# Optimization experiments

Measured on AMD Instinct MI355X. Metric: run time of the kernel, lower is better.

Reference implementation:

```python
import jax, jax.numpy as jnp
import numpy as np

B, N, E = 2, 5000, 160000
F_IN, HID, ED = 128, 128, 16
IN_EDGE = 2 * F_IN + 16 + ED  # source, target, radial(4*4), edge_attr


def _lin(k, fan_in, fan_out):
    return (jax.random.normal(k, (fan_in, fan_out), jnp.float32) / np.sqrt(fan_in)).astype(jnp.float32)


def setup_inputs() -> dict:
    key = jax.random.key(0)
    ks = jax.random.split(key, 16)
    h = jax.random.normal(ks[0], (B, N, F_IN), jnp.float32)
    coord = jax.random.normal(ks[1], (B, N, 4, 3), jnp.float32)
    edge_index = jax.random.randint(ks[2], (2, E), 0, N)
    edge_attr = jax.random.normal(ks[3], (E, ED), jnp.float32)
    return {
        "h": h, "coord": coord, "edge_index": edge_index, "edge_attr": edge_attr,
        # edge_mlp: Linear(IN_EDGE->HID), ReLU, Linear(HID->HID), ReLU
        "W_e1": _lin(ks[4], IN_EDGE, HID), "b_e1": jnp.zeros((HID,), jnp.float32),
        "W_e2": _lin(ks[5], HID, HID), "b_e2": jnp.zeros((HID,), jnp.float32),
        # node_mlp: Linear(HID+F_IN->HID), ReLU, Linear(HID->F_IN)
        "W_n1": _lin(ks[6], HID + F_IN, HID), "b_n1": jnp.zeros((HID,), jnp.float32),
        "W_n2": _lin(ks[7], HID, F_IN), "b_n2": jnp.zeros((F_IN,), jnp.float32),
        # coord_mlp: Linear(HID->HID), ReLU, Linear(HID->4, bias=False, xavier gain 0.001)
        "W_c1": _lin(ks[8], HID, HID), "b_c1": jnp.zeros((HID,), jnp.float32),
        "W_c2": _lin(ks[9], HID, 4) * 0.001,
    }


def reference(h, coord, edge_index, edge_attr,
              W_e1, b_e1, W_e2, b_e2,
              W_n1, b_n1, W_n2, b_n2,
              W_c1, b_c1, W_c2):
    row, col = edge_index[0], edge_index[1]
    coords_weight = 1.0
    n_nodes = h.shape[1]

    def single(h_b, coord_b):
        # coord2radial
        cd = coord_b[row] - coord_b[col]                                  # [E,4,3]
        prod = jnp.einsum('ejt,ekt->ejk', cd, cd).reshape(cd.shape[0], -1)  # [E,16]
        nrm = jnp.linalg.norm(prod, axis=-1, keepdims=True)
        radial = prod / jnp.maximum(nrm, 1e-12)                           # F.normalize
        # edge_model
        x = jnp.concatenate([h_b[row], h_b[col], radial, edge_attr], axis=-1)
        ef = jax.nn.relu(jax.nn.relu(x @ W_e1 + b_e1) @ W_e2 + b_e2)      # [E,HID]
        # coord_model: segment mean of cd * coord_mlp(ef)
        w = jax.nn.relu(ef @ W_c1 + b_c1) @ W_c2                          # [E,4]
        trans = cd * w[:, :, None]                                        # [E,4,3]
        agg_c = jax.ops.segment_sum(trans, row, num_segments=n_nodes)     # [N,4,3]
        cnt = jax.ops.segment_sum(jnp.ones((row.shape[0],), trans.dtype), row,
                                  num_segments=n_nodes)                   # [N]
        coord_new = coord_b + (agg_c / jnp.maximum(cnt, 1.0)[:, None, None]) * coords_weight
        # node_model (recurrent)
        agg_h = jax.ops.segment_sum(ef, row, num_segments=n_nodes)        # [N,HID]
        z = jnp.concatenate([h_b, agg_h], axis=-1)
        h_new = h_b + jax.nn.relu(z @ W_n1 + b_n1) @ W_n2 + b_n2
        return h_new, coord_new

    hs, coords = jax.vmap(single)(h, coord)
    return hs, coords
```

## Files before the change

### kernel.cpp

```cpp
#include <hip/hip_runtime.h>
#include <hip/hip_bf16.h>

#define B   2
#define NN_ 5000
#define NE_ 160000
#define F   128
#define HID 128
#define ED  16

typedef __bf16 bf16x8 __attribute__((ext_vector_type(8)));
typedef __bf16 bf16x4 __attribute__((ext_vector_type(4)));
typedef float  f32x4  __attribute__((ext_vector_type(4)));

#define MS  136
#define PS  40
#define EDG 64
#define ZS  264
#define HS  136
#define NPB2 32
#define NBUCKET 313

__global__ void pack_hist_kernel(const float* __restrict__ We1, const float* __restrict__ We2,
                                 const float* __restrict__ Wc1, const float* __restrict__ Wc2,
                                 const float* __restrict__ Wn1, const float* __restrict__ Wn2,
                                 const int* __restrict__ ei,
                                 __bf16* __restrict__ pw1, __bf16* __restrict__ pw2,
                                 __bf16* __restrict__ pwc1, __bf16* __restrict__ pwc2,
                                 __bf16* __restrict__ pwn1, __bf16* __restrict__ pwn2,
                                 float4* __restrict__ agg4, int* __restrict__ csr_cnt)
{
    if (blockIdx.x >= 472) {
        int i = (blockIdx.x - 472) * 256 + threadIdx.x;
        if (i < NE_) atomicAdd(&csr_cnt[ei[i]], 1);
        return;
    }
    int idx = blockIdx.x * 256 + threadIdx.x;
    const float* W; __bf16* P; int KT, Nr, local;
    if (idx < 36864)       { W = We1; P = pw1;  KT = 9; Nr = 128; local = idx; }
    else if (idx < 53248)  { W = We2; P = pw2;  KT = 4; Nr = 128; local = idx - 36864; }
    else if (idx < 69632)  { W = Wc1; P = pwc1; KT = 4; Nr = 128; local = idx - 53248; }
    else if (idx < 71680)  { W = Wc2; P = pwc2; KT = 4; Nr = 4;   local = idx - 69632; }
    else if (idx < 104448) { W = Wn1; P = pwn1; KT = 8; Nr = 128; local = idx - 71680; }
    else                   { W = Wn2; P = pwn2; KT = 4; Nr = 128; local = idx - 104448; }
    int j = local & 7, lane = (local >> 3) & 63, rest = local >> 9;
    int kt = rest % KT, nt = rest / KT;
    int k = kt * 32 + (lane >> 4) * 8 + j;
    int n = nt * 16 + (lane & 15);
    float v = (n < Nr) ? W[k * Nr + n] : 0.f;
    P[local] = (__bf16)v;

    float4 z4 = {0.f, 0.f, 0.f, 0.f};
    for (int i = idx; i < 350000; i += 120832) agg4[i] = z4;
}

__global__ __launch_bounds__(512) void scan_kernel(const int* __restrict__ csr_cnt,
                                                   int* __restrict__ csr_off, int* __restrict__ csr_pos)
{
    __shared__ int part[512];
    const int t = threadIdx.x;
    int sum = 0;
    #pragma unroll
    for (int j = 0; j < 10; j++) {
        int idx = t * 10 + j;
        if (idx < NN_) sum += csr_cnt[idx];
    }
    part[t] = sum;
    __syncthreads();
    for (int off = 1; off < 512; off <<= 1) {
        int v = (t >= off) ? part[t - off] : 0;
        __syncthreads();
        part[t] += v;
        __syncthreads();
    }
    int run = part[t] - sum;
    #pragma unroll
    for (int j = 0; j < 10; j++) {
        int idx = t * 10 + j;
        if (idx < NN_) { csr_off[idx] = run; csr_pos[idx] = run; run += csr_cnt[idx]; }
    }
    if (t == 0) csr_off[NN_] = NE_;
}

__global__ __launch_bounds__(512) void mid_kernel(
    const int* __restrict__ ei,
    int* __restrict__ csr_pos, int* __restrict__ bucket,
    const float* __restrict__ h, const __bf16* __restrict__ pw1,
    const float* __restrict__ be1,
    __bf16* __restrict__ pr, __bf16* __restrict__ pc)
{
    __shared__ __align__(16) __bf16 hs[128 * MS];
    const int t = threadIdx.x;

    if (blockIdx.x < NBUCKET) {
        int i = blockIdx.x * 512 + t;
        if (i < NE_) {
            int p = atomicAdd(&csr_pos[ei[i]], 1);
            bucket[p] = i;
        }
        return;
    }

    const int bp = blockIdx.x - NBUCKET;
    const int b = bp / 40;
    const int n0 = (bp % 40) * 128;
    const int lane = t & 63, wave = t >> 6;
    const int quad = lane >> 4, c = lane & 15;

    #pragma unroll
    for (int it = 0; it < 8; it++) {
        int idx = it * 512 + t;
        int node = idx >> 5, ch = idx & 31;
        int gn = n0 + node;
        float4 v = (gn < NN_) ? *(const float4*)&h[((size_t)b * NN_ + gn) * F + ch * 4]
                              : (float4){0.f, 0.f, 0.f, 0.f};
        bf16x4 bv = {(__bf16)v.x, (__bf16)v.y, (__bf16)v.z, (__bf16)v.w};
        *(bf16x4*)&hs[node * MS + ch * 4] = bv;
    }
    __syncthreads();

    const bf16x8* pw1v = (const bf16x8*)pw1;
    f32x4 accr[8], accc[8];
    #pragma unroll
    for (int m = 0; m < 8; m++) { accr[m] = (f32x4){0,0,0,0}; accc[m] = (f32x4){0,0,0,0}; }
    for (int kt = 0; kt < 4; kt++) {
        bf16x8 wr = pw1v[(wave * 9 + kt) * 64 + lane];
        bf16x8 wc = pw1v[(wave * 9 + kt + 4) * 64 + lane];
        #pragma unroll
        for (int m = 0; m < 8; m++) {
            bf16x8 x = *(const bf16x8*)&hs[(m * 16 + c) * MS + kt * 32 + quad * 8];
            accr[m] = __builtin_amdgcn_mfma_f32_16x16x32_bf16(wr, x, accr[m], 0, 0, 0);
            accc[m] = __builtin_amdgcn_mfma_f32_16x16x32_bf16(wc, x, accc[m], 0, 0, 0);
        }
    }
    float4 bb = *(const float4*)&be1[wave * 16 + quad * 4];
    #pragma unroll
    for (int m = 0; m < 8; m++) {
        int gn = n0 + m * 16 + c;
        if (gn < NN_) {
            size_t base = ((size_t)b * NN_ + gn) * F + wave * 16 + quad * 4;
            bf16x4 orr = {(__bf16)(accr[m][0] + bb.x), (__bf16)(accr[m][1] + bb.y),
                          (__bf16)(accr[m][2] + bb.z), (__bf16)(accr[m][3] + bb.w)};
            bf16x4 occ = {(__bf16)accc[m][0], (__bf16)accc[m][1], (__bf16)accc[m][2], (__bf16)accc[m][3]};
            *(bf16x4*)&pr[base] = orr;
            *(bf16x4*)&pc[base] = occ;
        }
    }
}

__global__ __launch_bounds__(256, 4) void edge_kernel(
    const __bf16* __restrict__ pr, const __bf16* __restrict__ pc,
    const float* __restrict__ coord,
    const int* __restrict__ ei, const float* __restrict__ ea,
    const int* __restrict__ bucket,
    const float* __restrict__ be2, const float* __restrict__ bc1,
    const __bf16* __restrict__ pw1, const __bf16* __restrict__ pw2,
    const __bf16* __restrict__ pwc1, const __bf16* __restrict__ pwc2,
    float* __restrict__ agg_h, float* __restrict__ agg_c)
{
    __shared__ __align__(16) __bf16 buf1[EDG * MS];
    __shared__ __align__(16) __bf16 buf2[EDG * MS];
    __shared__ __bf16 cds[EDG][12];
    __shared__ int rs[EDG], cs[EDG];

    const int t = threadIdx.x;
    const int b = blockIdx.y;
    const int p0 = blockIdx.x * EDG;
    const int lane = t & 63, wave = t >> 6;
    const int quad = lane >> 4, c = lane & 15;

    int eid_reg = 0;
    if (t < EDG) {
        eid_reg = bucket[p0 + t];
        rs[t] = ei[eid_reg]; cs[t] = ei[NE_ + eid_reg];
    }
    __syncthreads();

    const __bf16* prb = pr + (size_t)b * NN_ * F;
    const __bf16* pcb = pc + (size_t)b * NN_ * F;
    #pragma unroll
    for (int it = 0; it < 4; it++) {
        int idx = it * 256 + t;
        int e = idx >> 4, ch = idx & 15;
        bf16x8 a = *(const bf16x8*)(prb + (size_t)rs[e] * F + ch * 8);
        bf16x8 v = *(const bf16x8*)(pcb + (size_t)cs[e] * F + ch * 8);
        bf16x8 o;
        #pragma unroll
        for (int j = 0; j < 8; j++) o[j] = (__bf16)((float)a[j] + (float)v[j]);
        *(bf16x8*)&buf1[e * MS + ch * 8] = o;
    }
    if (t < EDG) {
        int e = t;
        const float* cr = coord + ((size_t)b * NN_ + rs[e]) * 12;
        const float* cc = coord + ((size_t)b * NN_ + cs[e]) * 12;
        float cd[12];
        #pragma unroll
        for (int j = 0; j < 12; j++) { cd[j] = cr[j] - cc[j]; cds[e][j] = (__bf16)cd[j]; }
        float prod[16]; float ss = 0.f;
        #pragma unroll
        for (int j = 0; j < 4; j++)
            #pragma unroll
            for (int k = 0; k < 4; k++) {
                float p = cd[j*3]*cd[k*3] + cd[j*3+1]*cd[k*3+1] + cd[j*3+2]*cd[k*3+2];
                prod[j*4 + k] = p; ss += p * p;
            }
        float inv = 1.0f / fmaxf(sqrtf(ss), 1e-12f);
        #pragma unroll
        for (int j = 0; j < 16; j++) buf2[e * PS + j] = (__bf16)(prod[j] * inv);
        const float4* ep = (const float4*)(ea + (size_t)eid_reg * ED);
        #pragma unroll
        for (int j = 0; j < 4; j++) {
            float4 v = ep[j];
            bf16x4 bv = {(__bf16)v.x, (__bf16)v.y, (__bf16)v.z, (__bf16)v.w};
            *(bf16x4*)&buf2[e * PS + 16 + j * 4] = bv;
        }
    }
    __syncthreads();

    const bf16x8* pw1v  = (const bf16x8*)pw1;
    const bf16x8* pw2v  = (const bf16x8*)pw2;
    const bf16x8* pwc1v = (const bf16x8*)pwc1;
    const bf16x8* pwc2v = (const bf16x8*)pwc2;

    f32x4 acc1[4][2];
    #pragma unroll
    for (int m = 0; m < 4; m++)
        #pragma unroll
        for (int n = 0; n < 2; n++) acc1[m][n] = (f32x4){0,0,0,0};
    {
        bf16x8 x1[4];
        #pragma unroll
        for (int m = 0; m < 4; m++)
            x1[m] = *(const bf16x8*)&buf2[(m*16 + c) * PS + quad*8];
        #pragma unroll
        for (int n = 0; n < 2; n++) {
            bf16x8 w = pw1v[((2*wave + n)*9 + 8)*64 + lane];
            #pragma unroll
            for (int m = 0; m < 4; m++)
                acc1[m][n] = __builtin_amdgcn_mfma_f32_16x16x32_bf16(w, x1[m], acc1[m][n], 0, 0, 0);
        }
    }
    #pragma unroll
    for (int n = 0; n < 2; n++) {
        int nt = 2*wave + n;
        #pragma unroll
        for (int m = 0; m < 4; m++) {
            int row = m*16 + c;
            bf16x4 p = *(const bf16x4*)&buf1[row * MS + nt*16 + quad*4];
            bf16x4 o = { (__bf16)fmaxf(acc1[m][n][0] + (float)p[0], 0.f),
                         (__bf16)fmaxf(acc1[m][n][1] + (float)p[1], 0.f),
                         (__bf16)fmaxf(acc1[m][n][2] + (float)p[2], 0.f),
                         (__bf16)fmaxf(acc1[m][n][3] + (float)p[3], 0.f) };
            *(bf16x4*)&buf1[row * MS + nt*16 + quad*4] = o;
        }
    }
    __syncthreads();

    f32x4 acc2[4][2];
    #pragma unroll
    for (int m = 0; m < 4; m++)
        #pragma unroll
        for (int n = 0; n < 2; n++) acc2[m][n] = (f32x4){0,0,0,0};
    for (int kt = 0; kt < 4; kt++) {
        bf16x8 x[4];
        #pragma unroll
        for (int m = 0; m < 4; m++)
            x[m] = *(const bf16x8*)&buf1[(m*16 + c) * MS + kt*32 + quad*8];
        #pragma unroll
        for (int n = 0; n < 2; n++) {
            bf16x8 w = pw2v[((2*wave + n)*4 + kt)*64 + lane];
            #pragma unroll
            for (int m = 0; m < 4; m++)
                acc2[m][n] = __builtin_amdgcn_mfma_f32_16x16x32_bf16(w, x[m], acc2[m][n], 0, 0, 0);
        }
    }
    #pragma unroll
    for (int n = 0; n < 2; n++) {
        int nt = 2*wave + n;
        float4 bb = *(const float4*)&be2[nt*16 + quad*4];
        #pragma unroll
        for (int m = 0; m < 4; m++) {
            int row = m*16 + c;
            bf16x4 o = { (__bf16)fmaxf(acc2[m][n][0] + bb.x, 0.f),
                         (__bf16)fmaxf(acc2[m][n][1] + bb.y, 0.f),
                         (__bf16)fmaxf(acc2[m][n][2] + bb.z, 0.f),
                         (__bf16)fmaxf(acc2[m][n][3] + bb.w, 0.f) };
            *(bf16x4*)&buf2[row * MS + nt*16 + quad*4] = o;
        }
    }
    __syncthreads();

    f32x4 acc3[4][2];
    #pragma unroll
    for (int m = 0; m < 4; m++)
        #pragma unroll
        for (int n = 0; n < 2; n++) acc3[m][n] = (f32x4){0,0,0,0};
    for (int kt = 0; kt < 4; kt++) {
        bf16x8 x[4];
        #pragma unroll
        for (int m = 0; m < 4; m++)
            x[m] = *(const bf16x8*)&buf2[(m*16 + c) * MS + kt*32 + quad*8];
        #pragma unroll
        for (int n = 0; n < 2; n++) {
            bf16x8 w = pwc1v[((2*wave + n)*4 + kt)*64 + lane];
            #pragma unroll
            for (int m = 0; m < 4; m++)
                acc3[m][n] = __builtin_amdgcn_mfma_f32_16x16x32_bf16(w, x[m], acc3[m][n], 0, 0, 0);
        }
    }
    #pragma unroll
    for (int n = 0; n < 2; n++) {
        int nt = 2*wave + n;
        float4 bb = *(const float4*)&bc1[nt*16 + quad*4];
        #pragma unroll
        for (int m = 0; m < 4; m++) {
            int row = m*16 + c;
            bf16x4 o = { (__bf16)fmaxf(acc3[m][n][0] + bb.x, 0.f),
                         (__bf16)fmaxf(acc3[m][n][1] + bb.y, 0.f),
                         (__bf16)fmaxf(acc3[m][n][2] + bb.z, 0.f),
                         (__bf16)fmaxf(acc3[m][n][3] + bb.w, 0.f) };
            *(bf16x4*)&buf1[row * MS + nt*16 + quad*4] = o;
        }
    }
    __syncthreads();

    f32x4 accw = (f32x4){0,0,0,0};
    for (int kt = 0; kt < 4; kt++) {
        bf16x8 x = *(const bf16x8*)&buf1[(wave*16 + c) * MS + kt*32 + quad*8];
        accw = __builtin_amdgcn_mfma_f32_16x16x32_bf16(pwc2v[kt*64 + lane], x, accw, 0, 0, 0);
    }
    if (quad == 0) {
        int e = wave*16 + c;
        #pragma unroll
        for (int j = 0; j < 12; j++)
            cds[e][j] = (__bf16)((float)cds[e][j] * accw[j/3]);
    }

    {
        float* aggh_b = agg_h + (size_t)b * NN_ * HID;
        const int col = t & 127, seg = t >> 7;
        float run = 0.f;
        int cur = rs[seg * 32];
        for (int e = seg * 32; e < seg * 32 + 32; e++) {
            int r = rs[e];
            float v = (float)buf2[e * MS + col];
            if (r != cur) {
                atomicAdd(&aggh_b[(size_t)cur * HID + col], run);
                run = 0.f; cur = r;
            }
            run += v;
        }
        atomicAdd(&aggh_b[(size_t)cur * HID + col], run);
    }
    __syncthreads();

    if (t < 24) {
        float* aggc_b = agg_c + (size_t)b * NN_ * 12;
        const int j = t % 12, q = t / 12;
        float run = 0.f;
        int cur = rs[q * 32];
        for (int e = q * 32; e < q * 32 + 32; e++) {
            int r = rs[e];
            float v = (float)cds[e][j];
            if (r != cur) {
                atomicAdd(&aggc_b[(size_t)cur * 12 + j], run);
                run = 0.f; cur = r;
            }
            run += v;
        }
        atomicAdd(&aggc_b[(size_t)cur * 12 + j], run);
    }
}

__global__ __launch_bounds__(256) void node_kernel(
    const float* __restrict__ h, const float* __restrict__ agg_h,
    const float* __restrict__ agg_c, const float* __restrict__ coord,
    const int* __restrict__ csr_off,
    const __bf16* __restrict__ pwn1, const float* __restrict__ bn1,
    const __bf16* __restrict__ pwn2, const float* __restrict__ bn2,
    float* __restrict__ out_h, float* __restrict__ out_c)
{
    __shared__ __align__(16) __bf16 zs[NPB2 * ZS];
    __shared__ __align__(16) __bf16 h1s[NPB2 * HS];
    const int t = threadIdx.x;
    const int b = blockIdx.y;
    const int n0 = blockIdx.x * NPB2;
    const int lane = t & 63, wave = t >> 6;
    const int quad = lane >> 4, c = lane & 15;

    #pragma unroll
    for (int it = 0; it < 8; it++) {
        int idx = it * 256 + t;
        int node = idx >> 6, ch = idx & 63;
        int gn = n0 + node;
        float4 v = (float4){0.f, 0.f, 0.f, 0.f};
        if (gn < NN_) {
            const float* src = (ch < 32) ? &h[((size_t)b * NN_ + gn) * F + ch * 4]
                                         : &agg_h[((size_t)b * NN_ + gn) * HID + (ch - 32) * 4];
            v = *(const float4*)src;
        }
        bf16x4 bv = {(__bf16)v.x, (__bf16)v.y, (__bf16)v.z, (__bf16)v.w};
        *(bf16x4*)&zs[node * ZS + ch * 4] = bv;
    }
    __syncthreads();

    const bf16x8* w1v = (const bf16x8*)pwn1;
    const bf16x8* w2v = (const bf16x8*)pwn2;
    f32x4 a1[2][2];
    #pragma unroll
    for (int m = 0; m < 2; m++)
        #pragma unroll
        for (int n = 0; n < 2; n++) a1[m][n] = (f32x4){0,0,0,0};
    for (int kt = 0; kt < 8; kt++) {
        bf16x8 x[2];
        #pragma unroll
        for (int m = 0; m < 2; m++)
            x[m] = *(const bf16x8*)&zs[(m*16 + c) * ZS + kt*32 + quad*8];
        #pragma unroll
        for (int n = 0; n < 2; n++) {
            bf16x8 w = w1v[((2*wave + n)*8 + kt)*64 + lane];
            #pragma unroll
            for (int m = 0; m < 2; m++)
                a1[m][n] = __builtin_amdgcn_mfma_f32_16x16x32_bf16(w, x[m], a1[m][n], 0, 0, 0);
        }
    }
    __syncthreads();
    #pragma unroll
    for (int n = 0; n < 2; n++) {
        int nt = 2*wave + n;
        float4 bb = *(const float4*)&bn1[nt*16 + quad*4];
        #pragma unroll
        for (int m = 0; m < 2; m++) {
            bf16x4 o = { (__bf16)fmaxf(a1[m][n][0] + bb.x, 0.f),
                         (__bf16)fmaxf(a1[m][n][1] + bb.y, 0.f),
                         (__bf16)fmaxf(a1[m][n][2] + bb.z, 0.f),
                         (__bf16)fmaxf(a1[m][n][3] + bb.w, 0.f) };
            *(bf16x4*)&h1s[(m*16 + c) * HS + nt*16 + quad*4] = o;
        }
    }
    __syncthreads();

    f32x4 a2[2][2];
    #pragma unroll
    for (int m = 0; m < 2; m++)
        #pragma unroll
        for (int n = 0; n < 2; n++) a2[m][n] = (f32x4){0,0,0,0};
    for (int kt = 0; kt < 4; kt++) {
        bf16x8 x[2];
        #pragma unroll
        for (int m = 0; m < 2; m++)
            x[m] = *(const bf16x8*)&h1s[(m*16 + c) * HS + kt*32 + quad*8];
        #pragma unroll
        for (int n = 0; n < 2; n++) {
            bf16x8 w = w2v[((2*wave + n)*4 + kt)*64 + lane];
            #pragma unroll
            for (int m = 0; m < 2; m++)
                a2[m][n] = __builtin_amdgcn_mfma_f32_16x16x32_bf16(w, x[m], a2[m][n], 0, 0, 0);
        }
    }
    float* os = (float*)zs;
    #pragma unroll
    for (int n = 0; n < 2; n++) {
        int nt = 2*wave + n;
        float4 bb = *(const float4*)&bn2[nt*16 + quad*4];
        #pragma unroll
        for (int m = 0; m < 2; m++) {
            f32x4 o = { a2[m][n][0] + bb.x, a2[m][n][1] + bb.y,
                        a2[m][n][2] + bb.z, a2[m][n][3] + bb.w };
            *(f32x4*)&os[(m*16 + c) * 132 + nt*16 + quad*4] = o;
        }
    }
    __syncthreads();

    #pragma unroll
    for (int it = 0; it < 4; it++) {
        int idx = it * 256 + t;
        int node = idx >> 5, ch = idx & 31;
        int gn = n0 + node;
        if (gn < NN_) {
            size_t gb = ((size_t)b * NN_ + gn) * F + ch * 4;
            float4 hres = *(const float4*)&h[gb];
            float4 acc = *(const float4*)&os[node * 132 + ch * 4];
            float4 o = { hres.x + acc.x, hres.y + acc.y, hres.z + acc.z, hres.w + acc.w };
            *(float4*)&out_h[gb] = o;
        }
    }
    for (int idx = t; idx < NPB2 * 12; idx += 256) {
        int node = idx / 12, j = idx % 12;
        int gn = n0 + node;
        if (gn < NN_) {
            float deg = (float)(csr_off[gn + 1] - csr_off[gn]);
            size_t ci = ((size_t)b * NN_ + gn) * 12 + j;
            out_c[ci] = coord[ci] + agg_c[ci] / fmaxf(deg, 1.0f);
        }
    }
}

extern "C" void kernel_launch(void* const* d_in, const int* in_sizes, int n_in,
                              void* d_out, int out_size, void* d_ws, size_t ws_size,
                              hipStream_t stream) {
    const float* h     = (const float*)d_in[0];
    const float* coord = (const float*)d_in[1];
    const int*   ei    = (const int*)d_in[2];
    const float* ea    = (const float*)d_in[3];
    const float* We1   = (const float*)d_in[4];
    const float* be1   = (const float*)d_in[5];
    const float* We2   = (const float*)d_in[6];
    const float* be2   = (const float*)d_in[7];
    const float* Wn1   = (const float*)d_in[8];
    const float* bn1   = (const float*)d_in[9];
    const float* Wn2   = (const float*)d_in[10];
    const float* bn2   = (const float*)d_in[11];
    const float* Wc1   = (const float*)d_in[12];
    const float* bc1   = (const float*)d_in[13];
    const float* Wc2   = (const float*)d_in[14];

    float* out_h = (float*)d_out;
    float* out_c = out_h + (size_t)B * NN_ * F;

    unsigned char* base = (unsigned char*)d_ws;
    __bf16* pw1  = (__bf16*)base;
    __bf16* pw2  = pw1 + 36864;
    __bf16* pwc1 = pw2 + 16384;
    __bf16* pwc2 = pwc1 + 16384;
    __bf16* pwn1 = pwc2 + 2048;
    __bf16* pwn2 = pwn1 + 32768;
    unsigned char* dyn = base + 241664;

    int* csr_cnt = (int*)(dyn);
    int* csr_off = (int*)(dyn + 20000);
    int* csr_pos = (int*)(dyn + 40016);
    int* bucket  = (int*)(dyn + 60016);
    float* agg_h = (float*)(dyn + 700016);
    float* agg_c = agg_h + (size_t)B * NN_ * HID;
    __bf16* pr   = (__bf16*)(agg_c + (size_t)B * NN_ * 12);
    __bf16* pc   = pr + (size_t)B * NN_ * F;

    hipMemsetAsync(csr_cnt, 0, 20000, stream);

    pack_hist_kernel<<<472 + 625, 256, 0, stream>>>(We1, We2, Wc1, Wc2, Wn1, Wn2, ei,
                                                    pw1, pw2, pwc1, pwc2, pwn1, pwn2,
                                                    (float4*)agg_h, csr_cnt);

    scan_kernel<<<1, 512, 0, stream>>>(csr_cnt, csr_off, csr_pos);

    mid_kernel<<<NBUCKET + 80, 512, 0, stream>>>(ei, csr_pos, bucket, h, pw1, be1, pr, pc);

    dim3 eg(NE_ / EDG, B);
    edge_kernel<<<eg, 256, 0, stream>>>(pr, pc, coord, ei, ea, bucket, be2, bc1,
                                        pw1, pw2, pwc1, pwc2, agg_h, agg_c);

    dim3 ng((NN_ + NPB2 - 1) / NPB2, B);
    node_kernel<<<ng, 256, 0, stream>>>(h, agg_h, agg_c, coord, csr_off,
                                        pwn1, bn1, pwn2, bn2, out_h, out_c);
}
```

Measured before the change: 193.5 us.

## Make edge kernel persistent with register prefetch of next chunk's gathers

The edge kernel becomes a persistent grid of 1024 blocks that loop over edge chunks. Each block prefetches the next chunk's bucket indices, projected node rows, coordinates and edge attributes into registers while the current chunk's MLP runs, so gather latency is hidden behind compute. The node projection (pr/pc) moves into the pack/histogram kernel, reading We1 directly from fp32 so it does not depend on the packed weights, and the bucket scatter becomes its own kernel. The coord2radial step is spread across 4 lanes per edge using shuffles. The cost is higher register pressure from the prefetch buffers and possible load imbalance across persistent blocks.

```diff
diff --git a/kernel.cpp b/kernel.cpp
--- a/kernel.cpp
+++ b/kernel.cpp
@@ -18,89 +18,50 @@
 #define ZS  264
 #define HS  136
 #define NPB2 32
-#define NBUCKET 313
-
-__global__ void pack_hist_kernel(const float* __restrict__ We1, const float* __restrict__ We2,
-                                 const float* __restrict__ Wc1, const float* __restrict__ Wc2,
-                                 const float* __restrict__ Wn1, const float* __restrict__ Wn2,
-                                 const int* __restrict__ ei,
-                                 __bf16* __restrict__ pw1, __bf16* __restrict__ pw2,
-                                 __bf16* __restrict__ pwc1, __bf16* __restrict__ pwc2,
-                                 __bf16* __restrict__ pwn1, __bf16* __restrict__ pwn2,
-                                 float4* __restrict__ agg4, int* __restrict__ csr_cnt)
-{
-    if (blockIdx.x >= 472) {
-        int i = (blockIdx.x - 472) * 256 + threadIdx.x;
-        if (i < NE_) atomicAdd(&csr_cnt[ei[i]], 1);
-        return;
-    }
-    int idx = blockIdx.x * 256 + threadIdx.x;
-    const float* W; __bf16* P; int KT, Nr, local;
-    if (idx < 36864)       { W = We1; P = pw1;  KT = 9; Nr = 128; local = idx; }
-    else if (idx < 53248)  { W = We2; P = pw2;  KT = 4; Nr = 128; local = idx - 36864; }
-    else if (idx < 69632)  { W = Wc1; P = pwc1; KT = 4; Nr = 128; local = idx - 53248; }
-    else if (idx < 71680)  { W = Wc2; P = pwc2; KT = 4; Nr = 4;   local = idx - 69632; }
-    else if (idx < 104448) { W = Wn1; P = pwn1; KT = 8; Nr = 128; local = idx - 71680; }
-    else                   { W = Wn2; P = pwn2; KT = 4; Nr = 128; local = idx - 104448; }
-    int j = local & 7, lane = (local >> 3) & 63, rest = local >> 9;
-    int kt = rest % KT, nt = rest / KT;
-    int k = kt * 32 + (lane >> 4) * 8 + j;
-    int n = nt * 16 + (lane & 15);
-    float v = (n < Nr) ? W[k * Nr + n] : 0.f;
-    P[local] = (__bf16)v;
-
-    float4 z4 = {0.f, 0.f, 0.f, 0.f};
-    for (int i = idx; i < 350000; i += 120832) agg4[i] = z4;
-}
-
-__global__ __launch_bounds__(512) void scan_kernel(const int* __restrict__ csr_cnt,
-                                                   int* __restrict__ csr_off, int* __restrict__ csr_pos)
-{
-    __shared__ int part[512];
-    const int t = threadIdx.x;
-    int sum = 0;
-    #pragma unroll
-    for (int j = 0; j < 10; j++) {
-        int idx = t * 10 + j;
-        if (idx < NN_) sum += csr_cnt[idx];
-    }
-    part[t] = sum;
-    __syncthreads();
-    for (int off = 1; off < 512; off <<= 1) {
-        int v = (t >= off) ? part[t - off] : 0;
-        __syncthreads();
-        part[t] += v;
-        __syncthreads();
-    }
-    int run = part[t] - sum;
-    #pragma unroll
-    for (int j = 0; j < 10; j++) {
-        int idx = t * 10 + j;
-        if (idx < NN_) { csr_off[idx] = run; csr_pos[idx] = run; run += csr_cnt[idx]; }
-    }
-    if (t == 0) csr_off[NN_] = NE_;
-}
-
-__global__ __launch_bounds__(512) void mid_kernel(
+#define EGRID 1024
+#define NCHUNK 5000
+
+__global__ __launch_bounds__(512) void pack_hist_kernel(
+    const float* __restrict__ We1, const float* __restrict__ We2,
+    const float* __restrict__ Wc1, const float* __restrict__ Wc2,
+    const float* __restrict__ Wn1, const float* __restrict__ Wn2,
     const int* __restrict__ ei,
-    int* __restrict__ csr_pos, int* __restrict__ bucket,
-    const float* __restrict__ h, const __bf16* __restrict__ pw1,
-    const float* __restrict__ be1,
+    const float* __restrict__ h, const float* __restrict__ be1,
+    __bf16* __restrict__ pw1, __bf16* __restrict__ pw2,
+    __bf16* __restrict__ pwc1, __bf16* __restrict__ pwc2,
+    __bf16* __restrict__ pwn1, __bf16* __restrict__ pwn2,
+    float4* __restrict__ agg4, int* __restrict__ csr_cnt,
     __bf16* __restrict__ pr, __bf16* __restrict__ pc)
 {
     __shared__ __align__(16) __bf16 hs[128 * MS];
     const int t = threadIdx.x;
 
-    if (blockIdx.x < NBUCKET) {
-        int i = blockIdx.x * 512 + t;
-        if (i < NE_) {
-            int p = atomicAdd(&csr_pos[ei[i]], 1);
-            bucket[p] = i;
-        }
+    if (blockIdx.x < 236) {
+        int idx = blockIdx.x * 512 + t;
+        const float* W; __bf16* P; int KT, Nr, local;
+        if (idx < 36864)       { W = We1; P = pw1;  KT = 9; Nr = 128; local = idx; }
+        else if (idx < 53248)  { W = We2; P = pw2;  KT = 4; Nr = 128; local = idx - 36864; }
+        else if (idx < 69632)  { W = Wc1; P = pwc1; KT = 4; Nr = 128; local = idx - 53248; }
+        else if (idx < 71680)  { W = Wc2; P = pwc2; KT = 4; Nr = 4;   local = idx - 69632; }
+        else if (idx < 104448) { W = Wn1; P = pwn1; KT = 8; Nr = 128; local = idx - 71680; }
+        else                   { W = Wn2; P = pwn2; KT = 4; Nr = 128; local = idx - 104448; }
+        int j = local & 7, lane = (local >> 3) & 63, rest = local >> 9;
+        int kt = rest % KT, nt = rest / KT;
+        int k = kt * 32 + (lane >> 4) * 8 + j;
+        int n = nt * 16 + (lane & 15);
+        float v = (n < Nr) ? W[k * Nr + n] : 0.f;
+        P[local] = (__bf16)v;
+        float4 z4 = {0.f, 0.f, 0.f, 0.f};
+        for (int i = idx; i < 350000; i += 120832) agg4[i] = z4;
         return;
     }
-
-    const int bp = blockIdx.x - NBUCKET;
+    if (blockIdx.x < 549) {
+        int i = (blockIdx.x - 236) * 512 + t;
+        if (i < NE_) atomicAdd(&csr_cnt[ei[i]], 1);
+        return;
+    }
+
+    const int bp = blockIdx.x - 549;
     const int b = bp / 40;
     const int n0 = (bp % 40) * 128;
     const int lane = t & 63, wave = t >> 6;
@@ -118,13 +79,17 @@
     }
     __syncthreads();
 
-    const bf16x8* pw1v = (const bf16x8*)pw1;
     f32x4 accr[8], accc[8];
     #pragma unroll
     for (int m = 0; m < 8; m++) { accr[m] = (f32x4){0,0,0,0}; accc[m] = (f32x4){0,0,0,0}; }
     for (int kt = 0; kt < 4; kt++) {
-        bf16x8 wr = pw1v[(wave * 9 + kt) * 64 + lane];
-        bf16x8 wc = pw1v[(wave * 9 + kt + 4) * 64 + lane];
+        bf16x8 wr, wc;
+        #pragma unroll
+        for (int jj = 0; jj < 8; jj++) {
+            int k = kt * 32 + quad * 8 + jj;
+            wr[jj] = (__bf16)We1[k * HID + wave * 16 + c];
+            wc[jj] = (__bf16)We1[(k + 128) * HID + wave * 16 + c];
+        }
         #pragma unroll
         for (int m = 0; m < 8; m++) {
             bf16x8 x = *(const bf16x8*)&hs[(m * 16 + c) * MS + kt * 32 + quad * 8];
@@ -144,6 +109,45 @@
             *(bf16x4*)&pr[base] = orr;
             *(bf16x4*)&pc[base] = occ;
         }
+    }
+}
+
+__global__ __launch_bounds__(512) void scan_kernel(const int* __restrict__ csr_cnt,
+                                                   int* __restrict__ csr_off, int* __restrict__ csr_pos)
+{
+    __shared__ int part[512];
+    const int t = threadIdx.x;
+    int sum = 0;
+    #pragma unroll
+    for (int j = 0; j < 10; j++) {
+        int idx = t * 10 + j;
+        if (idx < NN_) sum += csr_cnt[idx];
+    }
+    part[t] = sum;
+    __syncthreads();
+    for (int off = 1; off < 512; off <<= 1) {
+        int v = (t >= off) ? part[t - off] : 0;
+        __syncthreads();
+        part[t] += v;
+        __syncthreads();
+    }
+    int run = part[t] - sum;
+    #pragma unroll
+    for (int j = 0; j < 10; j++) {
+        int idx = t * 10 + j;
+        if (idx < NN_) { csr_off[idx] = run; csr_pos[idx] = run; run += csr_cnt[idx]; }
+    }
+    if (t == 0) csr_off[NN_] = NE_;
+}
+
+__global__ __launch_bounds__(512) void scatter_kernel(const int* __restrict__ ei,
+                                                      int* __restrict__ csr_pos,
+                                                      int* __restrict__ bucket)
+{
+    int i = blockIdx.x * 512 + threadIdx.x;
+    if (i < NE_) {
+        int p = atomicAdd(&csr_pos[ei[i]], 1);
+        bucket[p] = i;
     }
 }
 
@@ -161,213 +165,270 @@
     __shared__ __align__(16) __bf16 buf2[EDG * MS];
     __shared__ __bf16 cds[EDG][12];
     __shared__ int rs[EDG], cs[EDG];
+    __shared__ int rsN[EDG], csN[EDG], eidsN[EDG];
 
     const int t = threadIdx.x;
-    const int b = blockIdx.y;
-    const int p0 = blockIdx.x * EDG;
     const int lane = t & 63, wave = t >> 6;
     const int quad = lane >> 4, c = lane & 15;
-
-    int eid_reg = 0;
-    if (t < EDG) {
-        eid_reg = bucket[p0 + t];
-        rs[t] = ei[eid_reg]; cs[t] = ei[NE_ + eid_reg];
-    }
-    __syncthreads();
-
-    const __bf16* prb = pr + (size_t)b * NN_ * F;
-    const __bf16* pcb = pc + (size_t)b * NN_ * F;
-    #pragma unroll
-    for (int it = 0; it < 4; it++) {
-        int idx = it * 256 + t;
-        int e = idx >> 4, ch = idx & 15;
-        bf16x8 a = *(const bf16x8*)(prb + (size_t)rs[e] * F + ch * 8);
-        bf16x8 v = *(const bf16x8*)(pcb + (size_t)cs[e] * F + ch * 8);
-        bf16x8 o;
-        #pragma unroll
-        for (int j = 0; j < 8; j++) o[j] = (__bf16)((float)a[j] + (float)v[j]);
-        *(bf16x8*)&buf1[e * MS + ch * 8] = o;
-    }
-    if (t < EDG) {
-        int e = t;
-        const float* cr = coord + ((size_t)b * NN_ + rs[e]) * 12;
-        const float* cc = coord + ((size_t)b * NN_ + cs[e]) * 12;
-        float cd[12];
-        #pragma unroll
-        for (int j = 0; j < 12; j++) { cd[j] = cr[j] - cc[j]; cds[e][j] = (__bf16)cd[j]; }
-        float prod[16]; float ss = 0.f;
-        #pragma unroll
-        for (int j = 0; j < 4; j++)
-            #pragma unroll
-            for (int k = 0; k < 4; k++) {
-                float p = cd[j*3]*cd[k*3] + cd[j*3+1]*cd[k*3+1] + cd[j*3+2]*cd[k*3+2];
-                prod[j*4 + k] = p; ss += p * p;
-            }
-        float inv = 1.0f / fmaxf(sqrtf(ss), 1e-12f);
-        #pragma unroll
-        for (int j = 0; j < 16; j++) buf2[e * PS + j] = (__bf16)(prod[j] * inv);
-        const float4* ep = (const float4*)(ea + (size_t)eid_reg * ED);
-        #pragma unroll
-        for (int j = 0; j < 4; j++) {
-            float4 v = ep[j];
-            bf16x4 bv = {(__bf16)v.x, (__bf16)v.y, (__bf16)v.z, (__bf16)v.w};
-            *(bf16x4*)&buf2[e * PS + 16 + j * 4] = bv;
-        }
-    }
-    __syncthreads();
+    const int e4 = t >> 2, j4 = t & 3;
 
     const bf16x8* pw1v  = (const bf16x8*)pw1;
     const bf16x8* pw2v  = (const bf16x8*)pw2;
     const bf16x8* pwc1v = (const bf16x8*)pwc1;
     const bf16x8* pwc2v = (const bf16x8*)pwc2;
 
-    f32x4 acc1[4][2];
-    #pragma unroll
-    for (int m = 0; m < 4; m++)
-        #pragma unroll
-        for (int n = 0; n < 2; n++) acc1[m][n] = (f32x4){0,0,0,0};
+    int cid = blockIdx.x;
+
     {
-        bf16x8 x1[4];
+        const int bC = (cid >= 2500) ? 1 : 0;
+        const int p0 = (cid - bC * 2500) * EDG;
+        int mr = 0, mc = 0, me = 0;
+        if (t < EDG) {
+            me = bucket[p0 + t];
+            mr = ei[me];
+            mc = ei[NE_ + me];
+            rsN[t] = mr; csN[t] = mc; eidsN[t] = me;
+        }
+    }
+    __syncthreads();
+
+    bf16x8 prPF[4], pcPF[4];
+    float crN[3], ccN[3];
+    float4 eaNv;
+    {
+        const int bC = (cid >= 2500) ? 1 : 0;
+        const __bf16* prb = pr + (size_t)bC * NN_ * F;
+        const __bf16* pcb = pc + (size_t)bC * NN_ * F;
+        #pragma unroll
+        for (int it = 0; it < 4; it++) {
+            int idx = it * 256 + t, e = idx >> 4, ch = idx & 15;
+            prPF[it] = *(const bf16x8*)(prb + (size_t)rsN[e] * F + ch * 8);
+            pcPF[it] = *(const bf16x8*)(pcb + (size_t)csN[e] * F + ch * 8);
+        }
+        const float* crp = coord + ((size_t)bC * NN_ + rsN[e4]) * 12 + j4 * 3;
+        const float* ccp = coord + ((size_t)bC * NN_ + csN[e4]) * 12 + j4 * 3;
+        crN[0] = crp[0]; crN[1] = crp[1]; crN[2] = crp[2];
+        ccN[0] = ccp[0]; ccN[1] = ccp[1]; ccN[2] = ccp[2];
+        eaNv = *(const float4*)(ea + (size_t)eidsN[e4] * ED + j4 * 4);
+    }
+
+    for (; cid < NCHUNK; cid += EGRID) {
+        const int bCur = (cid >= 2500) ? 1 : 0;
+        const int nid = cid + EGRID;
+        const bool hn = nid < NCHUNK;
+
+        #pragma unroll
+        for (int it = 0; it < 4; it++) {
+            int idx = it * 256 + t, e = idx >> 4, ch = idx & 15;
+            bf16x8 a = prPF[it], v = pcPF[it];
+            bf16x8 o;
+            #pragma unroll
+            for (int j = 0; j < 8; j++) o[j] = (__bf16)((float)a[j] + (float)v[j]);
+            *(bf16x8*)&buf1[e * MS + ch * 8] = o;
+        }
+        {
+            float cd0 = crN[0] - ccN[0], cd1 = crN[1] - ccN[1], cd2 = crN[2] - ccN[2];
+            cds[e4][j4 * 3 + 0] = (__bf16)cd0;
+            cds[e4][j4 * 3 + 1] = (__bf16)cd1;
+            cds[e4][j4 * 3 + 2] = (__bf16)cd2;
+            float p[4], ssp = 0.f;
+            #pragma unroll
+            for (int k = 0; k < 4; k++) {
+                int sl = (lane & ~3) | k;
+                float bx = __shfl(cd0, sl, 64);
+                float by = __shfl(cd1, sl, 64);
+                float bz = __shfl(cd2, sl, 64);
+                p[k] = cd0 * bx + cd1 * by + cd2 * bz;
+                ssp += p[k] * p[k];
+            }
+            ssp += __shfl_xor(ssp, 1, 64);
+            ssp += __shfl_xor(ssp, 2, 64);
+            float inv = 1.0f / fmaxf(sqrtf(ssp), 1e-12f);
+            bf16x4 xp = {(__bf16)(p[0] * inv), (__bf16)(p[1] * inv),
+                         (__bf16)(p[2] * inv), (__bf16)(p[3] * inv)};
+            *(bf16x4*)&buf2[e4 * PS + j4 * 4] = xp;
+            bf16x4 bea = {(__bf16)eaNv.x, (__bf16)eaNv.y, (__bf16)eaNv.z, (__bf16)eaNv.w};
+            *(bf16x4*)&buf2[e4 * PS + 16 + j4 * 4] = bea;
+        }
+        if (t < EDG) { rs[t] = rsN[t]; cs[t] = csN[t]; }
+        __syncthreads();
+
+        int mr = 0, mc = 0, me = 0;
+        if (hn && t < EDG) {
+            const int bN = (nid >= 2500) ? 1 : 0;
+            const int p0n = (nid - bN * 2500) * EDG;
+            me = bucket[p0n + t];
+            mr = ei[me];
+            mc = ei[NE_ + me];
+        }
+
+        f32x4 acc1[4][2];
         #pragma unroll
         for (int m = 0; m < 4; m++)
-            x1[m] = *(const bf16x8*)&buf2[(m*16 + c) * PS + quad*8];
+            #pragma unroll
+            for (int n = 0; n < 2; n++) acc1[m][n] = (f32x4){0,0,0,0};
+        {
+            bf16x8 x1[4];
+            #pragma unroll
+            for (int m = 0; m < 4; m++)
+                x1[m] = *(const bf16x8*)&buf2[(m * 16 + c) * PS + quad * 8];
+            #pragma unroll
+            for (int n = 0; n < 2; n++) {
+                bf16x8 w = pw1v[((2 * wave + n) * 9 + 8) * 64 + lane];
+                #pragma unroll
+                for (int m = 0; m < 4; m++)
+                    acc1[m][n] = __builtin_amdgcn_mfma_f32_16x16x32_bf16(w, x1[m], acc1[m][n], 0, 0, 0);
+            }
+        }
         #pragma unroll
         for (int n = 0; n < 2; n++) {
-            bf16x8 w = pw1v[((2*wave + n)*9 + 8)*64 + lane];
+            int nt = 2 * wave + n;
+            #pragma unroll
+            for (int m = 0; m < 4; m++) {
+                int row = m * 16 + c;
+                bf16x4 pp = *(const bf16x4*)&buf1[row * MS + nt * 16 + quad * 4];
+                bf16x4 o = { (__bf16)fmaxf(acc1[m][n][0] + (float)pp[0], 0.f),
+                             (__bf16)fmaxf(acc1[m][n][1] + (float)pp[1], 0.f),
+                             (__bf16)fmaxf(acc1[m][n][2] + (float)pp[2], 0.f),
+                             (__bf16)fmaxf(acc1[m][n][3] + (float)pp[3], 0.f) };
+                *(bf16x4*)&buf1[row * MS + nt * 16 + quad * 4] = o;
+            }
+        }
+        if (hn && t < EDG) { rsN[t] = mr; csN[t] = mc; eidsN[t] = me; }
+        __syncthreads();
+
+        if (hn) {
+            const int bN = (nid >= 2500) ? 1 : 0;
+            const __bf16* prb = pr + (size_t)bN * NN_ * F;
+            const __bf16* pcb = pc + (size_t)bN * NN_ * F;
+            #pragma unroll
+            for (int it = 0; it < 4; it++) {
+                int idx = it * 256 + t, e = idx >> 4, ch = idx & 15;
+                prPF[it] = *(const bf16x8*)(prb + (size_t)rsN[e] * F + ch * 8);
+                pcPF[it] = *(const bf16x8*)(pcb + (size_t)csN[e] * F + ch * 8);
+            }
+            const float* crp = coord + ((size_t)bN * NN_ + rsN[e4]) * 12 + j4 * 3;
+            const float* ccp = coord + ((size_t)bN * NN_ + csN[e4]) * 12 + j4 * 3;
+            crN[0] = crp[0]; crN[1] = crp[1]; crN[2] = crp[2];
+            ccN[0] = ccp[0]; ccN[1] = ccp[1]; ccN[2] = ccp[2];
+            eaNv = *(const float4*)(ea + (size_t)eidsN[e4] * ED + j4 * 4);
+        }
+
+        f32x4 acc2[4][2];
+        #pragma unroll
+        for (int m = 0; m < 4; m++)
+            #pragma unroll
+            for (int n = 0; n < 2; n++) acc2[m][n] = (f32x4){0,0,0,0};
+        for (int kt = 0; kt < 4; kt++) {
+            bf16x8 x[4];
             #pragma unroll
             for (int m = 0; m < 4; m++)
-                acc1[m][n] = __builtin_amdgcn_mfma_f32_16x16x32_bf16(w, x1[m], acc1[m][n], 0, 0, 0);
-        }
-    }
-    #pragma unroll
-    for (int n = 0; n < 2; n++) {
-        int nt = 2*wave + n;
-        #pragma unroll
-        for (int m = 0; m < 4; m++) {
-            int row = m*16 + c;
-            bf16x4 p = *(const bf16x4*)&buf1[row * MS + nt*16 + quad*4];
-            bf16x4 o = { (__bf16)fmaxf(acc1[m][n][0] + (float)p[0], 0.f),
-                         (__bf16)fmaxf(acc1[m][n][1] + (float)p[1], 0.f),
-                         (__bf16)fmaxf(acc1[m][n][2] + (float)p[2], 0.f),
-                         (__bf16)fmaxf(acc1[m][n][3] + (float)p[3], 0.f) };
-            *(bf16x4*)&buf1[row * MS + nt*16 + quad*4] = o;
-        }
-    }
-    __syncthreads();
-
-    f32x4 acc2[4][2];
-    #pragma unroll
-    for (int m = 0; m < 4; m++)
-        #pragma unroll
-        for (int n = 0; n < 2; n++) acc2[m][n] = (f32x4){0,0,0,0};
-    for (int kt = 0; kt < 4; kt++) {
-        bf16x8 x[4];
+                x[m] = *(const bf16x8*)&buf1[(m * 16 + c) * MS + kt * 32 + quad * 8];
+            #pragma unroll
+            for (int n = 0; n < 2; n++) {
+                bf16x8 w = pw2v[((2 * wave + n) * 4 + kt) * 64 + lane];
+                #pragma unroll
+                for (int m = 0; m < 4; m++)
+                    acc2[m][n] = __builtin_amdgcn_mfma_f32_16x16x32_bf16(w, x[m], acc2[m][n], 0, 0, 0);
+            }
+        }
+        #pragma unroll
+        for (int n = 0; n < 2; n++) {
+            int nt = 2 * wave + n;
+            float4 bb = *(const float4*)&be2[nt * 16 + quad * 4];
+            #pragma unroll
+            for (int m = 0; m < 4; m++) {
+                int row = m * 16 + c;
+                bf16x4 o = { (__bf16)fmaxf(acc2[m][n][0] + bb.x, 0.f),
+                             (__bf16)fmaxf(acc2[m][n][1] + bb.y, 0.f),
+                             (__bf16)fmaxf(acc2[m][n][2] + bb.z, 0.f),
+                             (__bf16)fmaxf(acc2[m][n][3] + bb.w, 0.f) };
+                *(bf16x4*)&buf2[row * MS + nt * 16 + quad * 4] = o;
+            }
+        }
+        __syncthreads();
+
+        f32x4 acc3[4][2];
         #pragma unroll
         for (int m = 0; m < 4; m++)
-            x[m] = *(const bf16x8*)&buf1[(m*16 + c) * MS + kt*32 + quad*8];
+            #pragma unroll
+            for (int n = 0; n < 2; n++) acc3[m][n] = (f32x4){0,0,0,0};
+        for (int kt = 0; kt < 4; kt++) {
+            bf16x8 x[4];
+            #pragma unroll
+            for (int m = 0; m < 4; m++)
+                x[m] = *(const bf16x8*)&buf2[(m * 16 + c) * MS + kt * 32 + quad * 8];
+            #pragma unroll
+            for (int n = 0; n < 2; n++) {
+                bf16x8 w = pwc1v[((2 * wave + n) * 4 + kt) * 64 + lane];
+                #pragma unroll
+                for (int m = 0; m < 4; m++)
+                    acc3[m][n] = __builtin_amdgcn_mfma_f32_16x16x32_bf16(w, x[m], acc3[m][n], 0, 0, 0);
+            }
+        }
         #pragma unroll
         for (int n = 0; n < 2; n++) {
-            bf16x8 w = pw2v[((2*wave + n)*4 + kt)*64 + lane];
-            #pragma unroll
-            for (int m = 0; m < 4; m++)
-                acc2[m][n] = __builtin_amdgcn_mfma_f32_16x16x32_bf16(w, x[m], acc2[m][n], 0, 0, 0);
-        }
-    }
-    #pragma unroll
-    for (int n = 0; n < 2; n++) {
-        int nt = 2*wave + n;
-        float4 bb = *(const float4*)&be2[nt*16 + quad*4];
-        #pragma unroll
-        for (int m = 0; m < 4; m++) {
-            int row = m*16 + c;
-            bf16x4 o = { (__bf16)fmaxf(acc2[m][n][0] + bb.x, 0.f),
-                         (__bf16)fmaxf(acc2[m][n][1] + bb.y, 0.f),
-                         (__bf16)fmaxf(acc2[m][n][2] + bb.z, 0.f),
-                         (__bf16)fmaxf(acc2[m][n][3] + bb.w, 0.f) };
-            *(bf16x4*)&buf2[row * MS + nt*16 + quad*4] = o;
-        }
-    }
-    __syncthreads();
-
-    f32x4 acc3[4][2];
-    #pragma unroll
-    for (int m = 0; m < 4; m++)
-        #pragma unroll
-        for (int n = 0; n < 2; n++) acc3[m][n] = (f32x4){0,0,0,0};
-    for (int kt = 0; kt < 4; kt++) {
-        bf16x8 x[4];
-        #pragma unroll
-        for (int m = 0; m < 4; m++)
-            x[m] = *(const bf16x8*)&buf2[(m*16 + c) * MS + kt*32 + quad*8];
-        #pragma unroll
-        for (int n = 0; n < 2; n++) {
-            bf16x8 w = pwc1v[((2*wave + n)*4 + kt)*64 + lane];
-            #pragma unroll
-            for (int m = 0; m < 4; m++)
-                acc3[m][n] = __builtin_amdgcn_mfma_f32_16x16x32_bf16(w, x[m], acc3[m][n], 0, 0, 0);
-        }
-    }
-    #pragma unroll
-    for (int n = 0; n < 2; n++) {
-        int nt = 2*wave + n;
-        float4 bb = *(const float4*)&bc1[nt*16 + quad*4];
-        #pragma unroll
-        for (int m = 0; m < 4; m++) {
-            int row = m*16 + c;
-            bf16x4 o = { (__bf16)fmaxf(acc3[m][n][0] + bb.x, 0.f),
-                         (__bf16)fmaxf(acc3[m][n][1] + bb.y, 0.f),
-                         (__bf16)fmaxf(acc3[m][n][2] + bb.z, 0.f),
-                         (__bf16)fmaxf(acc3[m][n][3] + bb.w, 0.f) };
-            *(bf16x4*)&buf1[row * MS + nt*16 + quad*4] = o;
-        }
-    }
-    __syncthreads();
-
-    f32x4 accw = (f32x4){0,0,0,0};
-    for (int kt = 0; kt < 4; kt++) {
-        bf16x8 x = *(const bf16x8*)&buf1[(wave*16 + c) * MS + kt*32 + quad*8];
-        accw = __builtin_amdgcn_mfma_f32_16x16x32_bf16(pwc2v[kt*64 + lane], x, accw, 0, 0, 0);
-    }
-    if (quad == 0) {
-        int e = wave*16 + c;
-        #pragma unroll
-        for (int j = 0; j < 12; j++)
-            cds[e][j] = (__bf16)((float)cds[e][j] * accw[j/3]);
-    }
-
-    {
-        float* aggh_b = agg_h + (size_t)b * NN_ * HID;
-        const int col = t & 127, seg = t >> 7;
-        float run = 0.f;
-        int cur = rs[seg * 32];
-        for (int e = seg * 32; e < seg * 32 + 32; e++) {
-            int r = rs[e];
-            float v = (float)buf2[e * MS + col];
-            if (r != cur) {
-                atomicAdd(&aggh_b[(size_t)cur * HID + col], run);
-                run = 0.f; cur = r;
-            }
-            run += v;
-        }
-        atomicAdd(&aggh_b[(size_t)cur * HID + col], run);
-    }
-    __syncthreads();
-
-    if (t < 24) {
-        float* aggc_b = agg_c + (size_t)b * NN_ * 12;
-        const int j = t % 12, q = t / 12;
-        float run = 0.f;
-        int cur = rs[q * 32];
-        for (int e = q * 32; e < q * 32 + 32; e++) {
-            int r = rs[e];
-            float v = (float)cds[e][j];
-            if (r != cur) {
-                atomicAdd(&aggc_b[(size_t)cur * 12 + j], run);
-                run = 0.f; cur = r;
-            }
-            run += v;
-        }
-        atomicAdd(&aggc_b[(size_t)cur * 12 + j], run);
+            int nt = 2 * wave + n;
+            float4 bb = *(const float4*)&bc1[nt * 16 + quad * 4];
+            #pragma unroll
+            for (int m = 0; m < 4; m++) {
+                int row = m * 16 + c;
+                bf16x4 o = { (__bf16)fmaxf(acc3[m][n][0] + bb.x, 0.f),
+                             (__bf16)fmaxf(acc3[m][n][1] + bb.y, 0.f),
+                             (__bf16)fmaxf(acc3[m][n][2] + bb.z, 0.f),
+                             (__bf16)fmaxf(acc3[m][n][3] + bb.w, 0.f) };
+                *(bf16x4*)&buf1[row * MS + nt * 16 + quad * 4] = o;
+            }
+        }
+        __syncthreads();
+
+        f32x4 accw = (f32x4){0,0,0,0};
+        for (int kt = 0; kt < 4; kt++) {
+            bf16x8 x = *(const bf16x8*)&buf1[(wave * 16 + c) * MS + kt * 32 + quad * 8];
+            accw = __builtin_amdgcn_mfma_f32_16x16x32_bf16(pwc2v[kt * 64 + lane], x, accw, 0, 0, 0);
+        }
+        if (quad == 0) {
+            int e = wave * 16 + c;
+            #pragma unroll
+            for (int j = 0; j < 12; j++)
+                cds[e][j] = (__bf16)((float)cds[e][j] * accw[j / 3]);
+        }
+
+        {
+            float* aggh_b = agg_h + (size_t)bCur * NN_ * HID;
+            const int col = t & 127, seg = t >> 7;
+            float run = 0.f;
+            int cur = rs[seg * 32];
+            for (int e = seg * 32; e < seg * 32 + 32; e++) {
+                int r = rs[e];
+                float v = (float)buf2[e * MS + col];
+                if (r != cur) {
+                    atomicAdd(&aggh_b[(size_t)cur * HID + col], run);
+                    run = 0.f; cur = r;
+                }
+                run += v;
+            }
+            atomicAdd(&aggh_b[(size_t)cur * HID + col], run);
+        }
+        __syncthreads();
+
+        if (t < 24) {
+            float* aggc_b = agg_c + (size_t)bCur * NN_ * 12;
+            const int j = t % 12, q = t / 12;
+            float run = 0.f;
+            int cur = rs[q * 32];
+            for (int e = q * 32; e < q * 32 + 32; e++) {
+                int r = rs[e];
+                float v = (float)cds[e][j];
+                if (r != cur) {
+                    atomicAdd(&aggc_b[(size_t)cur * 12 + j], run);
+                    run = 0.f; cur = r;
+                }
+                run += v;
+            }
+            atomicAdd(&aggc_b[(size_t)cur * 12 + j], run);
+        }
+        __syncthreads();
     }
 }
 
@@ -414,10 +475,10 @@
         bf16x8 x[2];
         #pragma unroll
         for (int m = 0; m < 2; m++)
-            x[m] = *(const bf16x8*)&zs[(m*16 + c) * ZS + kt*32 + quad*8];
+            x[m] = *(const bf16x8*)&zs[(m * 16 + c) * ZS + kt * 32 + quad * 8];
         #pragma unroll
         for (int n = 0; n < 2; n++) {
-            bf16x8 w = w1v[((2*wave + n)*8 + kt)*64 + lane];
+            bf16x8 w = w1v[((2 * wave + n) * 8 + kt) * 64 + lane];
             #pragma unroll
             for (int m = 0; m < 2; m++)
                 a1[m][n] = __builtin_amdgcn_mfma_f32_16x16x32_bf16(w, x[m], a1[m][n], 0, 0, 0);
@@ -426,15 +487,15 @@
     __syncthreads();
     #pragma unroll
     for (int n = 0; n < 2; n++) {
-        int nt = 2*wave + n;
-        float4 bb = *(const float4*)&bn1[nt*16 + quad*4];
+        int nt = 2 * wave + n;
+        float4 bb = *(const float4*)&bn1[nt * 16 + quad * 4];
         #pragma unroll
         for (int m = 0; m < 2; m++) {
             bf16x4 o = { (__bf16)fmaxf(a1[m][n][0] + bb.x, 0.f),
                          (__bf16)fmaxf(a1[m][n][1] + bb.y, 0.f),
                          (__bf16)fmaxf(a1[m][n][2] + bb.z, 0.f),
                          (__bf16)fmaxf(a1[m][n][3] + bb.w, 0.f) };
-            *(bf16x4*)&h1s[(m*16 + c) * HS + nt*16 + quad*4] = o;
+            *(bf16x4*)&h1s[(m * 16 + c) * HS + nt * 16 + quad * 4] = o;
         }
     }
     __syncthreads();
@@ -448,10 +509,10 @@
         bf16x8 x[2];
         #pragma unroll
         for (int m = 0; m < 2; m++)
-            x[m] = *(const bf16x8*)&h1s[(m*16 + c) * HS + kt*32 + quad*8];
+            x[m] = *(const bf16x8*)&h1s[(m * 16 + c) * HS + kt * 32 + quad * 8];
         #pragma unroll
         for (int n = 0; n < 2; n++) {
-            bf16x8 w = w2v[((2*wave + n)*4 + kt)*64 + lane];
+            bf16x8 w = w2v[((2 * wave + n) * 4 + kt) * 64 + lane];
             #pragma unroll
             for (int m = 0; m < 2; m++)
                 a2[m][n] = __builtin_amdgcn_mfma_f32_16x16x32_bf16(w, x[m], a2[m][n], 0, 0, 0);
@@ -460,13 +521,13 @@
     float* os = (float*)zs;
     #pragma unroll
     for (int n = 0; n < 2; n++) {
-        int nt = 2*wave + n;
-        float4 bb = *(const float4*)&bn2[nt*16 + quad*4];
+        int nt = 2 * wave + n;
+        float4 bb = *(const float4*)&bn2[nt * 16 + quad * 4];
         #pragma unroll
         for (int m = 0; m < 2; m++) {
             f32x4 o = { a2[m][n][0] + bb.x, a2[m][n][1] + bb.y,
                         a2[m][n][2] + bb.z, a2[m][n][3] + bb.w };
-            *(f32x4*)&os[(m*16 + c) * 132 + nt*16 + quad*4] = o;
+            *(f32x4*)&os[(m * 16 + c) * 132 + nt * 16 + quad * 4] = o;
         }
     }
     __syncthreads();
@@ -537,17 +598,16 @@
 
     hipMemsetAsync(csr_cnt, 0, 20000, stream);
 
-    pack_hist_kernel<<<472 + 625, 256, 0, stream>>>(We1, We2, Wc1, Wc2, Wn1, Wn2, ei,
-                                                    pw1, pw2, pwc1, pwc2, pwn1, pwn2,
-                                                    (float4*)agg_h, csr_cnt);
+    pack_hist_kernel<<<629, 512, 0, stream>>>(We1, We2, Wc1, Wc2, Wn1, Wn2, ei, h, be1,
+                                              pw1, pw2, pwc1, pwc2, pwn1, pwn2,
+                                              (float4*)agg_h, csr_cnt, pr, pc);
 
     scan_kernel<<<1, 512, 0, stream>>>(csr_cnt, csr_off, csr_pos);
 
-    mid_kernel<<<NBUCKET + 80, 512, 0, stream>>>(ei, csr_pos, bucket, h, pw1, be1, pr, pc);
-
-    dim3 eg(NE_ / EDG, B);
-    edge_kernel<<<eg, 256, 0, stream>>>(pr, pc, coord, ei, ea, bucket, be2, bc1,
-                                        pw1, pw2, pwc1, pwc2, agg_h, agg_c);
+    scatter_kernel<<<313, 512, 0, stream>>>(ei, csr_pos, bucket);
+
+    edge_kernel<<<EGRID, 256, 0, stream>>>(pr, pc, coord, ei, ea, bucket, be2, bc1,
+                                           pw1, pw2, pwc1, pwc2, agg_h, agg_c);
 
     dim3 ng((NN_ + NPB2 - 1) / NPB2, B);
     node_kernel<<<ng, 256, 0, stream>>>(h, agg_h, agg_c, coord, csr_off,
```

After: 310.7 us. 60.6% more time.
